# Kernel optimization log

Hardware: AMD Instinct MI355X
Metric: run time of the kernel (lower is better)

## Reference

```python
import jax, jax.numpy as jnp
import numpy as np
import math

B, H, S, D = 2, 8, 512, 64

def setup_inputs() -> dict:
    key0 = jax.random.key(0)
    k1, k2, k3, k4, k5 = jax.random.split(key0, 5)
    return {
        "query": jax.random.normal(k1, (B, H, S, D), dtype=jnp.float32),
        "key":   jax.random.normal(k2, (B, H, S, D), dtype=jnp.float32),
        "value": jax.random.normal(k3, (B, H, S, D), dtype=jnp.float32),
        "R":     jax.random.normal(k4, (B, H, S, S, D), dtype=jnp.float32),
        "mask":  jax.random.randint(k5, (B, 1, S, S), 0, 2, dtype=jnp.int32),
    }

def reference(query, key, value, R, mask):
    d = query.shape[-1]
    # QK: [B,H,S,S]
    QK = jnp.einsum('bhqd,bhkd->bhqk', query, key)
    # QR: query . R per (q,k) pair -> [B,H,S,S]
    QR = jnp.einsum('bhqd,bhqkd->bhqk', query, R)
    scores = (QK + QR) / math.sqrt(d)
    neg = jnp.asarray(-1e9, scores.dtype)
    scores = jnp.where(mask == 0, neg, scores)
    p_attn = jax.nn.softmax(scores, axis=-1)
    p_attn = jnp.where(mask == 0, jnp.asarray(0.0, p_attn.dtype), p_attn)
    out = jnp.einsum('bhqk,bhkd->bhqd', p_attn, value)
    return out, p_attn
```

## Files before the change

kernel.cpp:

```cpp
#include <hip/hip_runtime.h>
#include <math.h>

#define Bb 2
#define Hh 8
#define Ss 512
#define Dd 64

typedef float floatx4 __attribute__((ext_vector_type(4)));

__global__ __launch_bounds__(256) void relattn_kernel(
    const float* __restrict__ Q, const float* __restrict__ Kmat,
    const float* __restrict__ V, const float* __restrict__ R,
    const int* __restrict__ mask, float* __restrict__ out,
    float* __restrict__ p_out)
{
    __shared__ float ssc_all[4][Ss];

    const int tid  = threadIdx.x;
    const int wave = tid >> 6;
    const int lane = tid & 63;
    float* ssc = ssc_all[wave];

    const int row = blockIdx.x * 4 + wave;
    const int q   = row & (Ss - 1);
    const int bh  = row >> 9;
    const int b   = bh >> 3;

    const int j  = lane & 15;
    const int kg = lane >> 4;

    const floatx4 qv = *(const floatx4*)(Q + (size_t)row * Dd + j * 4);
    const float* Rrow = R    + (size_t)row * Ss * Dd;
    const float* Kbh  = Kmat + (size_t)bh  * Ss * Dd;
    const float* Vbh  = V    + (size_t)bh  * Ss * Dd;

    #pragma unroll 4
    for (int k = kg; k < Ss; k += 4) {
        floatx4 rv = __builtin_nontemporal_load(
            (const floatx4*)(Rrow + k * Dd + j * 4));
        floatx4 kv = *(const floatx4*)(Kbh + k * Dd + j * 4);
        float p = qv.x * (rv.x + kv.x) + qv.y * (rv.y + kv.y)
                + qv.z * (rv.z + kv.z) + qv.w * (rv.w + kv.w);
        p += __shfl_xor(p, 1);
        p += __shfl_xor(p, 2);
        p += __shfl_xor(p, 4);
        p += __shfl_xor(p, 8);
        if (j == 0) ssc[k] = p * 0.125f;
    }
    __builtin_amdgcn_wave_barrier();

    const int* mrow = mask + (size_t)(b * Ss + q) * Ss;
    float s[8]; int m[8];
    #pragma unroll
    for (int i = 0; i < 8; ++i) {
        m[i] = mrow[lane + 64 * i];
        s[i] = ssc[lane + 64 * i];
        if (m[i] == 0) s[i] = -1e9f;
    }
    float mx = s[0];
    #pragma unroll
    for (int i = 1; i < 8; ++i) mx = fmaxf(mx, s[i]);
    #pragma unroll
    for (int o = 1; o < 64; o <<= 1) mx = fmaxf(mx, __shfl_xor(mx, o));

    float e[8], sm = 0.0f;
    #pragma unroll
    for (int i = 0; i < 8; ++i) { e[i] = __expf(s[i] - mx); sm += e[i]; }
    #pragma unroll
    for (int o = 1; o < 64; o <<= 1) sm += __shfl_xor(sm, o);
    const float inv = 1.0f / sm;

    float* prow = p_out + (size_t)row * Ss;
    #pragma unroll
    for (int i = 0; i < 8; ++i) {
        float p = (m[i] == 0) ? 0.0f : e[i] * inv;
        prow[lane + 64 * i] = p;
        ssc[lane + 64 * i]  = p;
    }
    __builtin_amdgcn_wave_barrier();

    floatx4 acc = {0.f, 0.f, 0.f, 0.f};
    #pragma unroll 4
    for (int k = kg; k < Ss; k += 4) {
        float pk = ssc[k];
        floatx4 vv = *(const floatx4*)(Vbh + k * Dd + j * 4);
        acc.x = fmaf(pk, vv.x, acc.x);
        acc.y = fmaf(pk, vv.y, acc.y);
        acc.z = fmaf(pk, vv.z, acc.z);
        acc.w = fmaf(pk, vv.w, acc.w);
    }
    #pragma unroll
    for (int o = 16; o <= 32; o <<= 1) {
        acc.x += __shfl_xor(acc.x, o);
        acc.y += __shfl_xor(acc.y, o);
        acc.z += __shfl_xor(acc.z, o);
        acc.w += __shfl_xor(acc.w, o);
    }
    if (kg == 0)
        *(floatx4*)(out + (size_t)row * Dd + j * 4) = acc;
}

extern "C" void kernel_launch(void* const* d_in, const int* in_sizes, int n_in,
                              void* d_out, int out_size, void* d_ws, size_t ws_size,
                              hipStream_t stream) {
    const float* Q    = (const float*)d_in[0];
    const float* K    = (const float*)d_in[1];
    const float* V    = (const float*)d_in[2];
    const float* R    = (const float*)d_in[3];
    const int*   mask = (const int*)d_in[4];

    float* out   = (float*)d_out;
    float* p_out = out + (size_t)Bb * Hh * Ss * Dd;

    relattn_kernel<<<(Bb * Hh * Ss) / 4, 256, 0, stream>>>(Q, K, V, R, mask, out, p_out);
}
```

Baseline: 1.319 ms.

## Compute each score per lane with wave-uniform query held in scalar registers

```diff
diff --git a/kernel.cpp b/kernel.cpp
--- a/kernel.cpp
+++ b/kernel.cpp
@@ -7,6 +7,10 @@
 #define Dd 64
 
 typedef float floatx4 __attribute__((ext_vector_type(4)));
+
+__device__ __forceinline__ float rfl(float x) {
+    return __int_as_float(__builtin_amdgcn_readfirstlane(__float_as_int(x)));
+}
 
 __global__ __launch_bounds__(256) void relattn_kernel(
     const float* __restrict__ Q, const float* __restrict__ Kmat,
@@ -21,42 +25,50 @@
     const int lane = tid & 63;
     float* ssc = ssc_all[wave];
 
-    const int row = blockIdx.x * 4 + wave;
+    const int row = __builtin_amdgcn_readfirstlane(blockIdx.x * 4 + wave);
     const int q   = row & (Ss - 1);
     const int bh  = row >> 9;
     const int b   = bh >> 3;
 
-    const int j  = lane & 15;
-    const int kg = lane >> 4;
+    float qs[Dd];
+    {
+        const floatx4* Q4 = (const floatx4*)(Q + (size_t)row * Dd);
+        #pragma unroll
+        for (int t = 0; t < 16; ++t) {
+            floatx4 v = Q4[t];
+            qs[4*t+0] = rfl(v.x); qs[4*t+1] = rfl(v.y);
+            qs[4*t+2] = rfl(v.z); qs[4*t+3] = rfl(v.w);
+        }
+    }
 
-    const floatx4 qv = *(const floatx4*)(Q + (size_t)row * Dd + j * 4);
+    const int* mrow = mask + (size_t)(b * Ss + q) * Ss;
+    int m[8];
+    #pragma unroll
+    for (int i = 0; i < 8; ++i) m[i] = mrow[lane + 64 * i];
+
     const float* Rrow = R    + (size_t)row * Ss * Dd;
     const float* Kbh  = Kmat + (size_t)bh  * Ss * Dd;
     const float* Vbh  = V    + (size_t)bh  * Ss * Dd;
 
-    #pragma unroll 4
-    for (int k = kg; k < Ss; k += 4) {
-        floatx4 rv = __builtin_nontemporal_load(
-            (const floatx4*)(Rrow + k * Dd + j * 4));
-        floatx4 kv = *(const floatx4*)(Kbh + k * Dd + j * 4);
-        float p = qv.x * (rv.x + kv.x) + qv.y * (rv.y + kv.y)
-                + qv.z * (rv.z + kv.z) + qv.w * (rv.w + kv.w);
-        p += __shfl_xor(p, 1);
-        p += __shfl_xor(p, 2);
-        p += __shfl_xor(p, 4);
-        p += __shfl_xor(p, 8);
-        if (j == 0) ssc[k] = p * 0.125f;
-    }
-    __builtin_amdgcn_wave_barrier();
-
-    const int* mrow = mask + (size_t)(b * Ss + q) * Ss;
-    float s[8]; int m[8];
+    float s[8];
     #pragma unroll
     for (int i = 0; i < 8; ++i) {
-        m[i] = mrow[lane + 64 * i];
-        s[i] = ssc[lane + 64 * i];
-        if (m[i] == 0) s[i] = -1e9f;
+        const int k = 64 * i + lane;
+        const floatx4* r4 = (const floatx4*)(Rrow + (size_t)k * Dd);
+        const floatx4* k4 = (const floatx4*)(Kbh  + (size_t)k * Dd);
+        float acc = 0.0f;
+        #pragma unroll
+        for (int t = 0; t < 16; ++t) {
+            floatx4 rv = __builtin_nontemporal_load(r4 + t);
+            floatx4 kv = k4[t];
+            acc = fmaf(rv.x + kv.x, qs[4*t+0], acc);
+            acc = fmaf(rv.y + kv.y, qs[4*t+1], acc);
+            acc = fmaf(rv.z + kv.z, qs[4*t+2], acc);
+            acc = fmaf(rv.w + kv.w, qs[4*t+3], acc);
+        }
+        s[i] = (m[i] == 0) ? -1e9f : acc * 0.125f;
     }
+
     float mx = s[0];
     #pragma unroll
     for (int i = 1; i < 8; ++i) mx = fmaxf(mx, s[i]);
@@ -79,11 +91,14 @@
     }
     __builtin_amdgcn_wave_barrier();
 
+    const int j  = lane & 15;
+    const int kg = lane >> 4;
+
     floatx4 acc = {0.f, 0.f, 0.f, 0.f};
     #pragma unroll 4
     for (int k = kg; k < Ss; k += 4) {
         float pk = ssc[k];
-        floatx4 vv = *(const floatx4*)(Vbh + k * Dd + j * 4);
+        floatx4 vv = *(const floatx4*)(Vbh + (size_t)k * Dd + j * 4);
         acc.x = fmaf(pk, vv.x, acc.x);
         acc.y = fmaf(pk, vv.y, acc.y);
         acc.z = fmaf(pk, vv.z, acc.z);
```

New measurement: 1.834 ms. 39.0% more time.
